# Optimization experiments

Hardware: AMD Instinct MI355X
Metric: run time of the kernel (lower is better)

## Reference

```python
import jax, jax.numpy as jnp
import numpy as np

N_NODES, N_EDGES = 16384, 8192
IN_CH, HID_CH = 256, 256
ALPHA, BETA = -1.5, -0.5


def setup_inputs() -> dict:
    key = jax.random.key(0)
    k1, k2, k3, k4, k5, k6 = jax.random.split(key, 6)
    x_0 = jax.random.normal(k1, (N_NODES, IN_CH), dtype=jnp.float32)
    # binary incidence matrix (n_nodes, n_edges)
    incidence_1 = jax.random.randint(k2, (N_NODES, N_EDGES), 0, 2).astype(jnp.float32)
    # conv weights (torch Conv: x @ W then neighborhood @ .)
    W0 = jax.random.normal(k3, (IN_CH, HID_CH), dtype=jnp.float32) * 0.02
    W1 = jax.random.normal(k4, (HID_CH, HID_CH), dtype=jnp.float32) * 0.02
    # xavier_uniform biases of shape (1, hidden)
    gain = 1.414
    bound = gain * np.sqrt(6.0 / (1 + HID_CH)) * np.sqrt(3.0) / np.sqrt(3.0)  # xavier bound = gain*sqrt(6/(fan_in+fan_out))
    bound = gain * np.sqrt(6.0 / (1 + HID_CH))
    bias_0_to_1 = jax.random.uniform(k5, (1, HID_CH), minval=-bound, maxval=bound, dtype=jnp.float32)
    bias_1_to_0 = jax.random.uniform(k6, (1, HID_CH), minval=-bound, maxval=bound, dtype=jnp.float32)
    return {"x_0": x_0, "incidence_1": incidence_1, "W0": W0, "W1": W1,
            "bias_0_to_1": bias_0_to_1, "bias_1_to_0": bias_1_to_0}


def _normalize_incidence(B1):
    # edge/node cardinalities raised to alpha/beta
    edge_card = jnp.sum(B1, axis=0) ** ALPHA          # (n_edges,)
    node_card = jnp.sum(B1, axis=1) ** BETA           # (n_nodes,)
    mask = (B1 > 0).astype(B1.dtype)
    d0_inv = 1.0 / (mask @ edge_card)                 # (n_nodes,) per-node sum of incident edge_card
    d1_inv = 1.0 / (mask.T @ node_card)               # (n_edges,) per-edge sum of member node_card
    # B1_norm = D0_left^-1 @ B1 @ diag(edge_card)
    B1_norm = d0_inv[:, None] * B1 * edge_card[None, :]
    # B1T_norm = D1_left^-1 @ B1^T @ diag(node_card)
    B1T_norm = d1_inv[:, None] * B1.T * node_card[None, :]
    return B1_norm, B1T_norm


def reference(x_0, incidence_1, W0, W1, bias_0_to_1, bias_1_to_0):
    B1_norm, B1T_norm = _normalize_incidence(incidence_1)
    # node -> edge conv: x_1 = B1T_norm @ (x_0 @ W0) + b01
    x_1 = B1T_norm @ (x_0 @ W0) + bias_0_to_1        # (n_edges, hid)
    # edge -> node conv: x_0 = B1_norm @ (x_1 @ W1) + b10
    x_0_out = B1_norm @ (x_1 @ W1) + bias_1_to_0     # (n_nodes, hid)
    return jax.nn.relu(x_0_out), jax.nn.relu(x_1)
```

## Files before the change

kernel.cpp:

```cpp
#include <hip/hip_runtime.h>
#include <stdint.h>

#define NN 16384
#define NE 8192
#define CH 256
#define MM1_SPLIT 8
#define MM2_SPLIT 4

typedef __attribute__((ext_vector_type(8))) short bf16x8;
typedef __attribute__((ext_vector_type(4))) float f32x4;

__device__ __forceinline__ unsigned short f2bf(float f) {
  unsigned u = __float_as_uint(f);
  u += 0x7FFFu + ((u >> 16) & 1u);
  return (unsigned short)(u >> 16);
}
__device__ __forceinline__ unsigned pack_trunc2(float a, float b) {
  return (__float_as_uint(b) & 0xFFFF0000u) | (__float_as_uint(a) >> 16);
}
__device__ __forceinline__ void async_copy16(const void* gptr, void* lptr) {
  __builtin_amdgcn_global_load_lds((const __attribute__((address_space(1))) unsigned int*)gptr,
                                   (__attribute__((address_space(3))) unsigned int*)lptr,
                                   16, 0, 0);
}

__global__ void k0_transpose_w(const float* __restrict__ W0, const float* __restrict__ W1,
                               unsigned short* __restrict__ W0T, unsigned short* __restrict__ W1T) {
  const float* W = blockIdx.y ? W1 : W0;
  unsigned short* WT = blockIdx.y ? W1T : W0T;
  int n = blockIdx.x;
  int k = threadIdx.x;
  WT[n * CH + k] = f2bf(W[k * CH + n]);
}

__global__ void k1_node_card(const float* __restrict__ B1, float* __restrict__ node_card) {
  int n = blockIdx.x;
  const float4* row = (const float4*)(B1 + (size_t)n * NE);
  float s = 0.f;
#pragma unroll
  for (int j = 0; j < 8; ++j) {
    float4 v = row[threadIdx.x + j * 256];
    s += v.x + v.y + v.z + v.w;
  }
  __shared__ float red[4];
#pragma unroll
  for (int off = 32; off; off >>= 1) s += __shfl_down(s, off, 64);
  if ((threadIdx.x & 63) == 0) red[threadIdx.x >> 6] = s;
  __syncthreads();
  if (threadIdx.x == 0) {
    float t = red[0] + red[1] + red[2] + red[3];
    node_card[n] = rsqrtf(t);
  }
}

__global__ __launch_bounds__(256) void k2_y0(const float* __restrict__ X0,
                                             const unsigned short* __restrict__ W0T,
                                             const float* __restrict__ node_card,
                                             unsigned short* __restrict__ y0sT) {
  __shared__ unsigned short a_lds[64 * 32];
  __shared__ unsigned short b_lds[256 * 32];
  const int tid = threadIdx.x;
  const int wave = tid >> 6, lane = tid & 63;
  const int quad = lane >> 4, l15 = lane & 15;
  const int m0 = blockIdx.x * 64;
  const int ar = tid >> 3, ac = (tid & 7) * 4;

  f32x4 acc[4][4];
  const f32x4 fz = {0.f, 0.f, 0.f, 0.f};
#pragma unroll
  for (int i = 0; i < 4; ++i)
#pragma unroll
    for (int j = 0; j < 4; ++j) acc[i][j] = fz;

  for (int k0 = 0; k0 < CH; k0 += 32) {
    __syncthreads();
#pragma unroll
    for (int p = 0; p < 2; ++p) {
      float4 v = *(const float4*)(X0 + (size_t)(m0 + ar + p * 32) * CH + k0 + ac);
      uint2 w;
      w.x = ((unsigned)f2bf(v.x)) | ((unsigned)f2bf(v.y) << 16);
      w.y = ((unsigned)f2bf(v.z)) | ((unsigned)f2bf(v.w) << 16);
      *(uint2*)&a_lds[(ar + p * 32) * 32 + ac] = w;
    }
#pragma unroll
    for (int i = 0; i < 4; ++i) {
      int rowbase = wave * 64 + i * 16;
      const unsigned short* g = W0T + (size_t)(rowbase + (lane >> 2)) * CH + k0 + (lane & 3) * 8;
      async_copy16(g, &b_lds[rowbase * 32]);
    }
    __syncthreads();
    bf16x8 af[4];
#pragma unroll
    for (int i = 0; i < 4; ++i)
      af[i] = *(const bf16x8*)&a_lds[(i * 16 + l15) * 32 + quad * 8];
#pragma unroll
    for (int j = 0; j < 4; ++j) {
      bf16x8 bfr = *(const bf16x8*)&b_lds[(wave * 64 + j * 16 + l15) * 32 + quad * 8];
#pragma unroll
      for (int i = 0; i < 4; ++i)
        acc[i][j] = __builtin_amdgcn_mfma_f32_16x16x32_bf16(af[i], bfr, acc[i][j], 0, 0, 0);
    }
  }
#pragma unroll
  for (int i = 0; i < 4; ++i) {
    int row4 = m0 + i * 16 + quad * 4;
    float4 nc = *(const float4*)(node_card + row4);
#pragma unroll
    for (int j = 0; j < 4; ++j) {
      int col = wave * 64 + j * 16 + l15;
      f32x4 v = acc[i][j];
      ushort4 o;
      o.x = f2bf(v[0] * nc.x);
      o.y = f2bf(v[1] * nc.y);
      o.z = f2bf(v[2] * nc.z);
      o.w = f2bf(v[3] * nc.w);
      *(ushort4*)&y0sT[(size_t)col * NN + row4] = o;
    }
  }
}

__global__ void k2b_aux(const float* __restrict__ node_card, unsigned short* __restrict__ y0sT) {
  int n = blockIdx.x * 256 + threadIdx.x;
  y0sT[(size_t)256 * NN + n] = f2bf(node_card[n]);
  y0sT[(size_t)257 * NN + n] = 0x3F80;
#pragma unroll
  for (int r = 258; r < 272; ++r) y0sT[(size_t)r * NN + n] = 0;
}

__global__ __launch_bounds__(256) void mm1_kernel(const float* __restrict__ B1,
                                                  const unsigned short* __restrict__ y0sT,
                                                  float* __restrict__ mm1p,
                                                  float* __restrict__ auxD,
                                                  float* __restrict__ auxC) {
  __shared__ unsigned short a_lds[64 * 40];
  __shared__ unsigned short b_lds[272 * 32];
  const int tid = threadIdx.x;
  const int wave = tid >> 6, lane = tid & 63;
  const int quad = lane >> 4, l15 = lane & 15;
  const int m0 = blockIdx.x * 64;
  const int sp = blockIdx.y;
  const int KS = NN / MM1_SPLIT;
  const int kbase = sp * KS;

  const int am4 = (tid & 15) * 4;
  const int anp = tid >> 4;
  const int ajb = anp >> 2, alow = anp & 3;

  f32x4 acc[4][4];
  f32x4 acc5[4];
  const f32x4 fz = {0.f, 0.f, 0.f, 0.f};
#pragma unroll
  for (int i = 0; i < 4; ++i) {
    acc5[i] = fz;
#pragma unroll
    for (int j = 0; j < 4; ++j) acc[i][j] = fz;
  }

  const float* agp = B1 + (size_t)(kbase + 2 * anp) * NE + m0 + am4;
  float4 va = *(const float4*)(agp);
  float4 vb = *(const float4*)(agp + NE);

  for (int kk = 0; kk < KS; kk += 32) {
    const int k0 = kbase + kk;
    __syncthreads();
    {
#pragma unroll
      for (int i = 0; i < 4; ++i) {
        int m = am4 + i;
        unsigned w = pack_trunc2(((const float*)&va)[i], ((const float*)&vb)[i]);
        int jbs = ajb ^ ((m >> 4) & 3);
        *(unsigned*)&a_lds[m * 40 + (jbs * 4 + alow) * 2] = w;
      }
    }
#pragma unroll
    for (int i = 0; i < 4; ++i) {
      int rowbase = wave * 64 + i * 16;
      const unsigned short* g = y0sT + (size_t)(rowbase + (lane >> 2)) * NN + k0 + (lane & 3) * 8;
      async_copy16(g, &b_lds[rowbase * 32]);
    }
    if (wave == 3) {
      const unsigned short* g = y0sT + (size_t)(256 + (lane >> 2)) * NN + k0 + (lane & 3) * 8;
      async_copy16(g, &b_lds[256 * 32]);
    }
    __syncthreads();
    if (kk + 32 < KS) {
      agp += (size_t)32 * NE;
      va = *(const float4*)(agp);
      vb = *(const float4*)(agp + NE);
    }
    bf16x8 af[4];
#pragma unroll
    for (int i = 0; i < 4; ++i) {
      int m = i * 16 + l15;
      int jbs = quad ^ ((m >> 4) & 3);
      af[i] = *(const bf16x8*)&a_lds[m * 40 + jbs * 8];
    }
#pragma unroll
    for (int j = 0; j < 4; ++j) {
      bf16x8 bfr = *(const bf16x8*)&b_lds[(wave * 64 + j * 16 + l15) * 32 + quad * 8];
#pragma unroll
      for (int i = 0; i < 4; ++i)
        acc[i][j] = __builtin_amdgcn_mfma_f32_16x16x32_bf16(af[i], bfr, acc[i][j], 0, 0, 0);
    }
    if (wave == 3) {
      bf16x8 bfr = *(const bf16x8*)&b_lds[(256 + l15) * 32 + quad * 8];
#pragma unroll
      for (int i = 0; i < 4; ++i)
        acc5[i] = __builtin_amdgcn_mfma_f32_16x16x32_bf16(af[i], bfr, acc5[i], 0, 0, 0);
    }
  }
  float* outp = mm1p + (size_t)sp * NE * CH;
#pragma unroll
  for (int i = 0; i < 4; ++i) {
    int row4 = m0 + i * 16 + quad * 4;
#pragma unroll
    for (int j = 0; j < 4; ++j) {
      int col = wave * 64 + j * 16 + l15;
#pragma unroll
      for (int r = 0; r < 4; ++r) outp[(size_t)(row4 + r) * CH + col] = acc[i][j][r];
    }
  }
  if (wave == 3 && l15 < 2) {
    float* dst = (l15 == 0 ? auxD : auxC) + (size_t)sp * NE;
#pragma unroll
    for (int i = 0; i < 4; ++i) {
      int row4 = m0 + i * 16 + quad * 4;
#pragma unroll
      for (int r = 0; r < 4; ++r) dst[row4 + r] = acc5[i][r];
    }
  }
}

__global__ void k3_edge_final(const float* __restrict__ mm1p, const float* __restrict__ auxD,
                              const float* __restrict__ auxC, const float* __restrict__ b01,
                              float* __restrict__ out1, unsigned short* __restrict__ x1bf,
                              float* __restrict__ edge_card) {
  int e = blockIdx.x, c = threadIdx.x;
  float ds = 0.f, p = 0.f;
#pragma unroll
  for (int sp = 0; sp < MM1_SPLIT; ++sp) {
    ds += auxD[(size_t)sp * NE + e];
    p += mm1p[(size_t)sp * NE * CH + (size_t)e * CH + c];
  }
  float x1 = p / ds + b01[c];
  out1[(size_t)e * CH + c] = fmaxf(x1, 0.f);
  x1bf[(size_t)e * CH + c] = f2bf(x1);
  if (c == 0) {
    float cs = 0.f;
#pragma unroll
    for (int sp = 0; sp < MM1_SPLIT; ++sp) cs += auxC[(size_t)sp * NE + e];
    edge_card[e] = 1.0f / (cs * sqrtf(cs));
  }
}

__global__ __launch_bounds__(256) void k5_y1(const unsigned short* __restrict__ x1bf,
                                             const unsigned short* __restrict__ W1T,
                                             const float* __restrict__ edge_card,
                                             unsigned short* __restrict__ y1sT) {
  __shared__ unsigned short a_lds[64 * 32];
  __shared__ unsigned short b_lds[256 * 32];
  const int tid = threadIdx.x;
  const int wave = tid >> 6, lane = tid & 63;
  const int quad = lane >> 4, l15 = lane & 15;
  const int m0 = blockIdx.x * 64;

  f32x4 acc[4][4];
  const f32x4 fz = {0.f, 0.f, 0.f, 0.f};
#pragma unroll
  for (int i = 0; i < 4; ++i)
#pragma unroll
    for (int j = 0; j < 4; ++j) acc[i][j] = fz;

  for (int k0 = 0; k0 < CH; k0 += 32) {
    __syncthreads();
    {
      const unsigned short* g = x1bf + (size_t)(m0 + wave * 16 + (lane >> 2)) * CH + k0 + (lane & 3) * 8;
      async_copy16(g, &a_lds[(wave * 16) * 32]);
    }
#pragma unroll
    for (int i = 0; i < 4; ++i) {
      int rowbase = wave * 64 + i * 16;
      const unsigned short* g = W1T + (size_t)(rowbase + (lane >> 2)) * CH + k0 + (lane & 3) * 8;
      async_copy16(g, &b_lds[rowbase * 32]);
    }
    __syncthreads();
    bf16x8 af[4];
#pragma unroll
    for (int i = 0; i < 4; ++i)
      af[i] = *(const bf16x8*)&a_lds[(i * 16 + l15) * 32 + quad * 8];
#pragma unroll
    for (int j = 0; j < 4; ++j) {
      bf16x8 bfr = *(const bf16x8*)&b_lds[(wave * 64 + j * 16 + l15) * 32 + quad * 8];
#pragma unroll
      for (int i = 0; i < 4; ++i)
        acc[i][j] = __builtin_amdgcn_mfma_f32_16x16x32_bf16(af[i], bfr, acc[i][j], 0, 0, 0);
    }
  }
#pragma unroll
  for (int i = 0; i < 4; ++i) {
    int row4 = m0 + i * 16 + quad * 4;
    float4 ec = *(const float4*)(edge_card + row4);
#pragma unroll
    for (int j = 0; j < 4; ++j) {
      int col = wave * 64 + j * 16 + l15;
      f32x4 v = acc[i][j];
      ushort4 o;
      o.x = f2bf(v[0] * ec.x);
      o.y = f2bf(v[1] * ec.y);
      o.z = f2bf(v[2] * ec.z);
      o.w = f2bf(v[3] * ec.w);
      *(ushort4*)&y1sT[(size_t)col * NE + row4] = o;
    }
  }
}

__global__ void k5b_aux(const float* __restrict__ edge_card, unsigned short* __restrict__ y1sT) {
  int e = blockIdx.x * 256 + threadIdx.x;
  y1sT[(size_t)256 * NE + e] = f2bf(edge_card[e]);
#pragma unroll
  for (int r = 257; r < 272; ++r) y1sT[(size_t)r * NE + e] = 0;
}

__global__ __launch_bounds__(256) void mm2_kernel(const float* __restrict__ B1,
                                                  const unsigned short* __restrict__ y1sT,
                                                  float* __restrict__ mm2p,
                                                  float* __restrict__ d0p) {
  __shared__ unsigned short a_lds[64 * 40];
  __shared__ unsigned short b_lds[272 * 32];
  const int tid = threadIdx.x;
  const int wave = tid >> 6, lane = tid & 63;
  const int quad = lane >> 4, l15 = lane & 15;
  const int m0 = blockIdx.x * 64;
  const int sp = blockIdx.y;
  const int KS = NE / MM2_SPLIT;
  const int kbase = sp * KS;
  const int ar = tid >> 3, ac = (tid & 7) * 4;

  f32x4 acc[4][4];
  f32x4 acc5[4];
  const f32x4 fz = {0.f, 0.f, 0.f, 0.f};
#pragma unroll
  for (int i = 0; i < 4; ++i) {
    acc5[i] = fz;
#pragma unroll
    for (int j = 0; j < 4; ++j) acc[i][j] = fz;
  }

  const float* agp = B1 + (size_t)(m0 + ar) * NE + kbase + ac;
  float4 va = *(const float4*)(agp);
  float4 vb = *(const float4*)(agp + (size_t)32 * NE);

  for (int kk = 0; kk < KS; kk += 32) {
    const int k0 = kbase + kk;
    __syncthreads();
    {
      uint2 w0, w1;
      w0.x = pack_trunc2(va.x, va.y);
      w0.y = pack_trunc2(va.z, va.w);
      w1.x = pack_trunc2(vb.x, vb.y);
      w1.y = pack_trunc2(vb.z, vb.w);
      *(uint2*)&a_lds[ar * 40 + ac] = w0;
      *(uint2*)&a_lds[(ar + 32) * 40 + ac] = w1;
    }
#pragma unroll
    for (int i = 0; i < 4; ++i) {
      int rowbase = wave * 64 + i * 16;
      const unsigned short* g = y1sT + (size_t)(rowbase + (lane >> 2)) * NE + k0 + (lane & 3) * 8;
      async_copy16(g, &b_lds[rowbase * 32]);
    }
    if (wave == 3) {
      const unsigned short* g = y1sT + (size_t)(256 + (lane >> 2)) * NE + k0 + (lane & 3) * 8;
      async_copy16(g, &b_lds[256 * 32]);
    }
    __syncthreads();
    if (kk + 32 < KS) {
      agp += 32;
      va = *(const float4*)(agp);
      vb = *(const float4*)(agp + (size_t)32 * NE);
    }
    bf16x8 af[4];
#pragma unroll
    for (int i = 0; i < 4; ++i)
      af[i] = *(const bf16x8*)&a_lds[(i * 16 + l15) * 40 + quad * 8];
#pragma unroll
    for (int j = 0; j < 4; ++j) {
      bf16x8 bfr = *(const bf16x8*)&b_lds[(wave * 64 + j * 16 + l15) * 32 + quad * 8];
#pragma unroll
      for (int i = 0; i < 4; ++i)
        acc[i][j] = __builtin_amdgcn_mfma_f32_16x16x32_bf16(af[i], bfr, acc[i][j], 0, 0, 0);
    }
    if (wave == 3) {
      bf16x8 bfr = *(const bf16x8*)&b_lds[(256 + l15) * 32 + quad * 8];
#pragma unroll
      for (int i = 0; i < 4; ++i)
        acc5[i] = __builtin_amdgcn_mfma_f32_16x16x32_bf16(af[i], bfr, acc5[i], 0, 0, 0);
    }
  }
  float* outp = mm2p + (size_t)sp * NN * CH;
#pragma unroll
  for (int i = 0; i < 4; ++i) {
    int row4 = m0 + i * 16 + quad * 4;
#pragma unroll
    for (int j = 0; j < 4; ++j) {
      int col = wave * 64 + j * 16 + l15;
#pragma unroll
      for (int r = 0; r < 4; ++r) outp[(size_t)(row4 + r) * CH + col] = acc[i][j][r];
    }
  }
  if (wave == 3 && l15 == 0) {
#pragma unroll
    for (int i = 0; i < 4; ++i) {
      int row4 = m0 + i * 16 + quad * 4;
#pragma unroll
      for (int r = 0; r < 4; ++r) d0p[(size_t)sp * NN + row4 + r] = acc5[i][r];
    }
  }
}

__global__ void k6_node_final(const float* __restrict__ mm2p, const float* __restrict__ d0p,
                              const float* __restrict__ b10, float* __restrict__ out0) {
  int n = blockIdx.x, c = threadIdx.x;
  float s = 0.f, d = 0.f;
#pragma unroll
  for (int sp = 0; sp < MM2_SPLIT; ++sp) {
    s += mm2p[(size_t)sp * NN * CH + (size_t)n * CH + c];
    d += d0p[(size_t)sp * NN + n];
  }
  float v = s / d + b10[c];
  out0[(size_t)n * CH + c] = fmaxf(v, 0.f);
}

extern "C" void kernel_launch(void* const* d_in, const int* in_sizes, int n_in,
                              void* d_out, int out_size, void* d_ws, size_t ws_size,
                              hipStream_t stream) {
  const float* x0 = (const float*)d_in[0];
  const float* B1 = (const float*)d_in[1];
  const float* W0 = (const float*)d_in[2];
  const float* W1 = (const float*)d_in[3];
  const float* b01 = (const float*)d_in[4];
  const float* b10 = (const float*)d_in[5];
  float* out0 = (float*)d_out;
  float* out1 = out0 + (size_t)NN * CH;

  char* ws = (char*)d_ws;
  size_t off = 0;
  auto take = [&](size_t bytes) {
    void* p = ws + off;
    off += (bytes + 255) & ~(size_t)255;
    return p;
  };
  unsigned short* y0sT = (unsigned short*)take((size_t)272 * NN * 2);
  unsigned short* y1sT = (unsigned short*)take((size_t)272 * NE * 2);
  unsigned short* x1bf = (unsigned short*)take((size_t)NE * CH * 2);
  float* mm1p = (float*)take((size_t)MM1_SPLIT * NE * CH * 4);
  float* mm2p = mm1p;
  float* node_card = (float*)take((size_t)NN * 4);
  float* edge_card = (float*)take((size_t)NE * 4);
  float* auxD = (float*)take((size_t)MM1_SPLIT * NE * 4);
  float* auxC = (float*)take((size_t)MM1_SPLIT * NE * 4);
  float* d0p = (float*)take((size_t)MM2_SPLIT * NN * 4);
  unsigned short* W0T = (unsigned short*)take((size_t)CH * CH * 2);
  unsigned short* W1T = (unsigned short*)take((size_t)CH * CH * 2);
  (void)ws_size; (void)in_sizes; (void)n_in; (void)out_size;

  k0_transpose_w<<<dim3(256, 2), 256, 0, stream>>>(W0, W1, W0T, W1T);
  k1_node_card<<<NN, 256, 0, stream>>>(B1, node_card);
  k2_y0<<<NN / 64, 256, 0, stream>>>(x0, W0T, node_card, y0sT);
  k2b_aux<<<NN / 256, 256, 0, stream>>>(node_card, y0sT);
  mm1_kernel<<<dim3(NE / 64, MM1_SPLIT), 256, 0, stream>>>(B1, y0sT, mm1p, auxD, auxC);
  k3_edge_final<<<NE, 256, 0, stream>>>(mm1p, auxD, auxC, b01, out1, x1bf, edge_card);
  k5_y1<<<NE / 64, 256, 0, stream>>>(x1bf, W1T, edge_card, y1sT);
  k5b_aux<<<NE / 256, 256, 0, stream>>>(edge_card, y1sT);
  mm2_kernel<<<dim3(NN / 64, MM2_SPLIT), 256, 0, stream>>>(B1, y1sT, mm2p, d0p);
  k6_node_final<<<NN, 256, 0, stream>>>(mm2p, d0p, b10, out0);
}
```

Measured before the change: 1.150 ms.

## Bit-pack incidence matrix once and feed both GEMMs from packed bits

```diff
diff --git a/kernel.cpp b/kernel.cpp
--- a/kernel.cpp
+++ b/kernel.cpp
@@ -15,13 +15,27 @@
   u += 0x7FFFu + ((u >> 16) & 1u);
   return (unsigned short)(u >> 16);
 }
-__device__ __forceinline__ unsigned pack_trunc2(float a, float b) {
-  return (__float_as_uint(b) & 0xFFFF0000u) | (__float_as_uint(a) >> 16);
-}
 __device__ __forceinline__ void async_copy16(const void* gptr, void* lptr) {
   __builtin_amdgcn_global_load_lds((const __attribute__((address_space(1))) unsigned int*)gptr,
                                    (__attribute__((address_space(3))) unsigned int*)lptr,
                                    16, 0, 0);
+}
+
+__device__ __forceinline__ void transpose32(unsigned* x) {
+  const unsigned masks[5] = {0x0000FFFFu, 0x00FF00FFu, 0x0F0F0F0Fu, 0x33333333u, 0x55555555u};
+#pragma unroll
+  for (int jj = 0; jj < 5; ++jj) {
+    const int j = 16 >> jj;
+    const unsigned m = masks[jj];
+#pragma unroll
+    for (int k = 0; k < 32; ++k) {
+      if ((k & j) == 0) {
+        unsigned t = ((x[k] >> j) ^ x[k + j]) & m;
+        x[k] ^= (t << j);
+        x[k + j] ^= t;
+      }
+    }
+  }
 }
 
 __global__ void k0_transpose_w(const float* __restrict__ W0, const float* __restrict__ W1,
@@ -33,23 +47,53 @@
   WT[n * CH + k] = f2bf(W[k * CH + n]);
 }
 
-__global__ void k1_node_card(const float* __restrict__ B1, float* __restrict__ node_card) {
+__global__ void k1_pack_card(const float* __restrict__ B1, unsigned* __restrict__ pk1,
+                             float* __restrict__ node_card) {
   int n = blockIdx.x;
-  const float4* row = (const float4*)(B1 + (size_t)n * NE);
-  float s = 0.f;
-#pragma unroll
-  for (int j = 0; j < 8; ++j) {
-    float4 v = row[threadIdx.x + j * 256];
-    s += v.x + v.y + v.z + v.w;
-  }
-  __shared__ float red[4];
+  int t = threadIdx.x;
+  const float4* p = (const float4*)(B1 + (size_t)n * NE + t * 32);
+  unsigned w = 0;
+#pragma unroll
+  for (int jj = 0; jj < 8; ++jj) {
+    float4 v = p[jj];
+    w |= ((__float_as_uint(v.x) >> 23) & 1u) << (4 * jj);
+    w |= ((__float_as_uint(v.y) >> 23) & 1u) << (4 * jj + 1);
+    w |= ((__float_as_uint(v.z) >> 23) & 1u) << (4 * jj + 2);
+    w |= ((__float_as_uint(v.w) >> 23) & 1u) << (4 * jj + 3);
+  }
+  pk1[(size_t)n * 256 + t] = w;
+  int s = __popc(w);
+  __shared__ int red[4];
 #pragma unroll
   for (int off = 32; off; off >>= 1) s += __shfl_down(s, off, 64);
-  if ((threadIdx.x & 63) == 0) red[threadIdx.x >> 6] = s;
+  if ((t & 63) == 0) red[t >> 6] = s;
   __syncthreads();
-  if (threadIdx.x == 0) {
-    float t = red[0] + red[1] + red[2] + red[3];
-    node_card[n] = rsqrtf(t);
+  if (t == 0) {
+    float tot = (float)(red[0] + red[1] + red[2] + red[3]);
+    node_card[n] = rsqrtf(tot);
+  }
+}
+
+__global__ __launch_bounds__(256) void k1b_bitT(const unsigned* __restrict__ pk1,
+                                                unsigned* __restrict__ pk1T) {
+  int bw = blockIdx.x & 127;
+  int half = blockIdx.x >> 7;
+  int t = threadIdx.x;
+  int nt = half * 256 + t;
+  unsigned x0[32], x1[32];
+#pragma unroll
+  for (int r = 0; r < 32; ++r) {
+    uint2 v = *(const uint2*)&pk1[(size_t)(nt * 32 + r) * 256 + 2 * bw];
+    x0[r] = v.x;
+    x1[r] = v.y;
+  }
+  transpose32(x0);
+  transpose32(x1);
+  int e0 = bw * 64;
+#pragma unroll
+  for (int c = 0; c < 32; ++c) {
+    pk1T[(size_t)(e0 + c) * 512 + nt] = x0[c];
+    pk1T[(size_t)(e0 + 32 + c) * 512 + nt] = x1[c];
   }
 }
 
@@ -57,8 +101,8 @@
                                              const unsigned short* __restrict__ W0T,
                                              const float* __restrict__ node_card,
                                              unsigned short* __restrict__ y0sT) {
-  __shared__ unsigned short a_lds[64 * 32];
-  __shared__ unsigned short b_lds[256 * 32];
+  __shared__ __align__(16) unsigned short a_lds[64 * 32];
+  __shared__ __align__(16) unsigned short b_lds[256 * 32];
   const int tid = threadIdx.x;
   const int wave = tid >> 6, lane = tid & 63;
   const int quad = lane >> 4, l15 = lane & 15;
@@ -127,13 +171,13 @@
   for (int r = 258; r < 272; ++r) y0sT[(size_t)r * NN + n] = 0;
 }
 
-__global__ __launch_bounds__(256) void mm1_kernel(const float* __restrict__ B1,
+__global__ __launch_bounds__(256) void mm1_kernel(const unsigned char* __restrict__ pk1T,
                                                   const unsigned short* __restrict__ y0sT,
                                                   float* __restrict__ mm1p,
                                                   float* __restrict__ auxD,
                                                   float* __restrict__ auxC) {
-  __shared__ unsigned short a_lds[64 * 40];
-  __shared__ unsigned short b_lds[272 * 32];
+  __shared__ __align__(16) unsigned short a_lds[64 * 40];
+  __shared__ __align__(16) unsigned short b_lds[272 * 32];
   const int tid = threadIdx.x;
   const int wave = tid >> 6, lane = tid & 63;
   const int quad = lane >> 4, l15 = lane & 15;
@@ -142,9 +186,10 @@
   const int KS = NN / MM1_SPLIT;
   const int kbase = sp * KS;
 
-  const int am4 = (tid & 15) * 4;
-  const int anp = tid >> 4;
-  const int ajb = anp >> 2, alow = anp & 3;
+  const int am = tid >> 2;
+  const int akg = tid & 3;
+  const int ajbs = akg ^ ((am >> 4) & 3);
+  unsigned short* aw_dst = &a_lds[am * 40 + ajbs * 8];
 
   f32x4 acc[4][4];
   f32x4 acc5[4];
@@ -156,21 +201,21 @@
     for (int j = 0; j < 4; ++j) acc[i][j] = fz;
   }
 
-  const float* agp = B1 + (size_t)(kbase + 2 * anp) * NE + m0 + am4;
-  float4 va = *(const float4*)(agp);
-  float4 vb = *(const float4*)(agp + NE);
+  const unsigned char* agp = pk1T + (size_t)(m0 + am) * (NN / 8) + (kbase >> 3) + akg;
+  unsigned abyte = *agp;
 
   for (int kk = 0; kk < KS; kk += 32) {
     const int k0 = kbase + kk;
     __syncthreads();
     {
-#pragma unroll
-      for (int i = 0; i < 4; ++i) {
-        int m = am4 + i;
-        unsigned w = pack_trunc2(((const float*)&va)[i], ((const float*)&vb)[i]);
-        int jbs = ajb ^ ((m >> 4) & 3);
-        *(unsigned*)&a_lds[m * 40 + (jbs * 4 + alow) * 2] = w;
+      uint4 aw;
+#pragma unroll
+      for (int j = 0; j < 4; ++j) {
+        unsigned lo = (abyte >> (2 * j)) & 1u;
+        unsigned hi = (abyte >> (2 * j + 1)) & 1u;
+        ((unsigned*)&aw)[j] = lo * 0x3F80u + hi * 0x3F800000u;
       }
+      *(uint4*)aw_dst = aw;
     }
 #pragma unroll
     for (int i = 0; i < 4; ++i) {
@@ -184,9 +229,8 @@
     }
     __syncthreads();
     if (kk + 32 < KS) {
-      agp += (size_t)32 * NE;
-      va = *(const float4*)(agp);
-      vb = *(const float4*)(agp + NE);
+      agp += 4;
+      abyte = *agp;
     }
     bf16x8 af[4];
 #pragma unroll
@@ -257,8 +301,8 @@
                                              const unsigned short* __restrict__ W1T,
                                              const float* __restrict__ edge_card,
                                              unsigned short* __restrict__ y1sT) {
-  __shared__ unsigned short a_lds[64 * 32];
-  __shared__ unsigned short b_lds[256 * 32];
+  __shared__ __align__(16) unsigned short a_lds[64 * 32];
+  __shared__ __align__(16) unsigned short b_lds[256 * 32];
   const int tid = threadIdx.x;
   const int wave = tid >> 6, lane = tid & 63;
   const int quad = lane >> 4, l15 = lane & 15;
@@ -321,12 +365,12 @@
   for (int r = 257; r < 272; ++r) y1sT[(size_t)r * NE + e] = 0;
 }
 
-__global__ __launch_bounds__(256) void mm2_kernel(const float* __restrict__ B1,
+__global__ __launch_bounds__(256) void mm2_kernel(const unsigned char* __restrict__ pk1,
                                                   const unsigned short* __restrict__ y1sT,
                                                   float* __restrict__ mm2p,
                                                   float* __restrict__ d0p) {
-  __shared__ unsigned short a_lds[64 * 40];
-  __shared__ unsigned short b_lds[272 * 32];
+  __shared__ __align__(16) unsigned short a_lds[64 * 40];
+  __shared__ __align__(16) unsigned short b_lds[272 * 32];
   const int tid = threadIdx.x;
   const int wave = tid >> 6, lane = tid & 63;
   const int quad = lane >> 4, l15 = lane & 15;
@@ -334,7 +378,10 @@
   const int sp = blockIdx.y;
   const int KS = NE / MM2_SPLIT;
   const int kbase = sp * KS;
-  const int ar = tid >> 3, ac = (tid & 7) * 4;
+
+  const int am = tid >> 2;
+  const int akg = tid & 3;
+  unsigned short* aw_dst = &a_lds[am * 40 + akg * 8];
 
   f32x4 acc[4][4];
   f32x4 acc5[4];
@@ -346,21 +393,21 @@
     for (int j = 0; j < 4; ++j) acc[i][j] = fz;
   }
 
-  const float* agp = B1 + (size_t)(m0 + ar) * NE + kbase + ac;
-  float4 va = *(const float4*)(agp);
-  float4 vb = *(const float4*)(agp + (size_t)32 * NE);
+  const unsigned char* agp = pk1 + (size_t)(m0 + am) * (NE / 8) + (kbase >> 3) + akg;
+  unsigned abyte = *agp;
 
   for (int kk = 0; kk < KS; kk += 32) {
     const int k0 = kbase + kk;
     __syncthreads();
     {
-      uint2 w0, w1;
-      w0.x = pack_trunc2(va.x, va.y);
-      w0.y = pack_trunc2(va.z, va.w);
-      w1.x = pack_trunc2(vb.x, vb.y);
-      w1.y = pack_trunc2(vb.z, vb.w);
-      *(uint2*)&a_lds[ar * 40 + ac] = w0;
-      *(uint2*)&a_lds[(ar + 32) * 40 + ac] = w1;
+      uint4 aw;
+#pragma unroll
+      for (int j = 0; j < 4; ++j) {
+        unsigned lo = (abyte >> (2 * j)) & 1u;
+        unsigned hi = (abyte >> (2 * j + 1)) & 1u;
+        ((unsigned*)&aw)[j] = lo * 0x3F80u + hi * 0x3F800000u;
+      }
+      *(uint4*)aw_dst = aw;
     }
 #pragma unroll
     for (int i = 0; i < 4; ++i) {
@@ -374,9 +421,8 @@
     }
     __syncthreads();
     if (kk + 32 < KS) {
-      agp += 32;
-      va = *(const float4*)(agp);
-      vb = *(const float4*)(agp + (size_t)32 * NE);
+      agp += 4;
+      abyte = *agp;
     }
     bf16x8 af[4];
 #pragma unroll
@@ -461,16 +507,19 @@
   float* d0p = (float*)take((size_t)MM2_SPLIT * NN * 4);
   unsigned short* W0T = (unsigned short*)take((size_t)CH * CH * 2);
   unsigned short* W1T = (unsigned short*)take((size_t)CH * CH * 2);
+  unsigned* pk1 = (unsigned*)take((size_t)NN * 256 * 4);
+  unsigned* pk1T = (unsigned*)take((size_t)NE * 512 * 4);
   (void)ws_size; (void)in_sizes; (void)n_in; (void)out_size;
 
   k0_transpose_w<<<dim3(256, 2), 256, 0, stream>>>(W0, W1, W0T, W1T);
-  k1_node_card<<<NN, 256, 0, stream>>>(B1, node_card);
+  k1_pack_card<<<NN, 256, 0, stream>>>(B1, pk1, node_card);
+  k1b_bitT<<<256, 256, 0, stream>>>(pk1, pk1T);
   k2_y0<<<NN / 64, 256, 0, stream>>>(x0, W0T, node_card, y0sT);
   k2b_aux<<<NN / 256, 256, 0, stream>>>(node_card, y0sT);
-  mm1_kernel<<<dim3(NE / 64, MM1_SPLIT), 256, 0, stream>>>(B1, y0sT, mm1p, auxD, auxC);
+  mm1_kernel<<<dim3(NE / 64, MM1_SPLIT), 256, 0, stream>>>((const unsigned char*)pk1T, y0sT, mm1p, auxD, auxC);
   k3_edge_final<<<NE, 256, 0, stream>>>(mm1p, auxD, auxC, b01, out1, x1bf, edge_card);
   k5_y1<<<NE / 64, 256, 0, stream>>>(x1bf, W1T, edge_card, y1sT);
   k5b_aux<<<NE / 256, 256, 0, stream>>>(edge_card, y1sT);
-  mm2_kernel<<<dim3(NN / 64, MM2_SPLIT), 256, 0, stream>>>(B1, y1sT, mm2p, d0p);
+  mm2_kernel<<<dim3(NN / 64, MM2_SPLIT), 256, 0, stream>>>((const unsigned char*)pk1, y1sT, mm2p, d0p);
   k6_node_final<<<NN, 256, 0, stream>>>(mm2p, d0p, b10, out0);
 }
```

Result: faster. 1.085 ms (-5.6%).
